# Performance work log

Measured on AMD Instinct MI355X. Metric: run time of the kernel, lower is better.

The kernel has to match this reference:

```python
import jax, jax.numpy as jnp
import numpy as np

EPS = 1e-5

def layer_norm(v, g, b):
    # torch LayerNorm: biased variance, eps inside sqrt
    m = v.mean(-1, keepdims=True)
    var = ((v - m) ** 2).mean(-1, keepdims=True)
    return (v - m) / jnp.sqrt(var + EPS) * g + b

def setup_inputs() -> dict:
    key = jax.random.key(0)
    k_q, k_x, k_w = jax.random.split(key, 3)
    B, C1, H, W = 8, 1024, 32, 32
    C2 = 32
    Cp = C1 // 4  # proj output dim = 256
    q = jax.random.normal(k_q, (B, C1, H, W), jnp.float32)
    x = jax.random.normal(k_x, (B, C2, H, W), jnp.float32)
    Wp = jax.random.normal(k_w, (Cp, C1), jnp.float32) / np.sqrt(C1).astype(np.float32)
    bp = jnp.zeros((Cp,), jnp.float32)
    g1 = jnp.ones((Cp,), jnp.float32)
    b1 = jnp.zeros((Cp,), jnp.float32)
    g2 = jnp.ones((C2,), jnp.float32)
    b2 = jnp.zeros((C2,), jnp.float32)
    return {"q": q, "x": x, "Wp": Wp, "bp": bp, "g1": g1, "b1": b1, "g2": g2, "b2": b2}

def reference(q, x, Wp, bp, g1, b1, g2, b2):
    B, C1, H, W = q.shape
    C2 = x.shape[1]
    Cp = Wp.shape[0]
    N = H * W
    qf = q.reshape(B, C1, N).transpose(0, 2, 1)   # [B, N, C1]
    xf = x.reshape(B, C2, N).transpose(0, 2, 1)   # [B, N, C2]
    qn = layer_norm(jnp.einsum('bnc,dc->bnd', qf, Wp) + bp, g1, b1)  # [B, N, Cp]
    xn = layer_norm(xf, g2, b2)                                      # [B, N, C2]
    out = jnp.einsum('bnc,bnd->bncd', qn, xn)     # [B, N, Cp, C2]
    out = out.reshape(B, N, Cp * C2).transpose(0, 2, 1).reshape(B, Cp * C2, H, W)
    return out
```

## Files before the change

kernel.cpp:

```cpp
#include <hip/hip_runtime.h>

typedef __attribute__((ext_vector_type(8))) short bf16x8;
typedef __attribute__((ext_vector_type(4))) float f32x4;

#define C1N 1024
#define CP 256
#define C2N 32
#define NPB 1024
#define BATCH 8
#define BK 64

__device__ __forceinline__ unsigned short f2bf(float f) {
  unsigned u = __float_as_uint(f);
  u += 0x7fffu + ((u >> 16) & 1u);
  return (unsigned short)(u >> 16);
}

__global__ __launch_bounds__(256) void prep_kernel(
    const float* __restrict__ x, const float* __restrict__ Wp,
    const float* __restrict__ g2, const float* __restrict__ b2,
    short* __restrict__ Wpb, float* __restrict__ xn)
{
  const int tid = threadIdx.x;
  if (blockIdx.x < 32) {
    int g = blockIdx.x * 256 + tid;
    int b = g >> 10, n = g & 1023;
    const float* xb = x + (size_t)b * C2N * NPB + n;
    float v[C2N];
    float s = 0.f;
#pragma unroll
    for (int c = 0; c < C2N; ++c) { v[c] = xb[(size_t)c * NPB]; s += v[c]; }
    float m = s * (1.0f / C2N);
    float s2 = 0.f;
#pragma unroll
    for (int c = 0; c < C2N; ++c) { float d = v[c] - m; s2 += d * d; }
    float rs = rsqrtf(s2 * (1.0f / C2N) + 1e-5f);
    float* xo = xn + (size_t)b * C2N * NPB + n;
#pragma unroll
    for (int c = 0; c < C2N; ++c) xo[(size_t)c * NPB] = (v[c] - m) * rs * g2[c] + b2[c];
  } else {
    int base = (blockIdx.x - 32) * 256 + tid;
#pragma unroll
    for (int it = 0; it < 8; ++it) {
      int pos = it * 8192 + base;
      f32x4 w = ((const f32x4*)Wp)[pos];
      ushort4 o;
      o.x = f2bf(w.x); o.y = f2bf(w.y); o.z = f2bf(w.z); o.w = f2bf(w.w);
      ((ushort4*)Wpb)[pos] = o;
    }
  }
}

__global__ __launch_bounds__(512) void gemm_ln_kernel(
    const float* __restrict__ q, const short* __restrict__ Wpb,
    const float* __restrict__ bp, const float* __restrict__ g1, const float* __restrict__ b1,
    float* __restrict__ qn)
{
  __shared__ short Wp_s[2][CP * BK];
  __shared__ float p1[8][32], p2[8][32], lm[32], lr[32];

  const int tid  = threadIdx.x;
  const int lane = tid & 63;
  const int wv   = tid >> 6;
  const int colA = lane & 15;
  const int grp  = lane >> 4;
  const int bb   = blockIdx.y;
  const int n0   = blockIdx.x * 32;

  const float* qb = q + (size_t)bb * C1N * NPB;

  f32x4 acc[2][2];
#pragma unroll
  for (int i = 0; i < 2; ++i)
#pragma unroll
    for (int j = 0; j < 2; ++j) acc[i][j] = (f32x4){0.f, 0.f, 0.f, 0.f};

  const int drow_off = lane >> 3;
  const int kslot_g  = (lane & 7) ^ drow_off;

  auto stage = [&](int buf, int ks) {
    const int k0 = ks * BK;
#pragma unroll
    for (int i = 0; i < 4; ++i) {
      int d0 = wv * 32 + i * 8;
      const short* gsrc = Wpb + (size_t)(d0 + drow_off) * C1N + k0 + kslot_g * 8;
      short* ldst = &Wp_s[buf][d0 * BK];
      __builtin_amdgcn_global_load_lds((const __attribute__((address_space(1))) void*)gsrc,
                                       (__attribute__((address_space(3))) void*)ldst,
                                       16, 0, 0);
    }
  };

  stage(0, 0);
  __syncthreads();

  for (int ks = 0; ks < C1N / BK; ++ks) {
    const int cur = ks & 1;
    if (ks < C1N / BK - 1) stage(cur ^ 1, ks + 1);

    const float* qk = qb + (size_t)(ks * BK) * NPB + n0;
#pragma unroll
    for (int kk2 = 0; kk2 < 2; ++kk2) {
      bf16x8 bfrag[2];
#pragma unroll
      for (int nf = 0; nf < 2; ++nf) {
#pragma unroll
        for (int j = 0; j < 8; ++j) {
          float v = qk[(size_t)(kk2 * 32 + grp * 8 + j) * NPB + nf * 16 + colA];
          bfrag[nf][j] = (short)f2bf(v);
        }
      }
#pragma unroll
      for (int df = 0; df < 2; ++df) {
        int row  = wv * 32 + df * 16 + colA;
        int boff = row * (BK * 2) + ((((kk2 << 2) + grp) ^ (row & 7)) << 4);
        bf16x8 afrag = *(const bf16x8*)((const char*)&Wp_s[cur][0] + boff);
        acc[df][0] = __builtin_amdgcn_mfma_f32_16x16x32_bf16(afrag, bfrag[0], acc[df][0], 0, 0, 0);
        acc[df][1] = __builtin_amdgcn_mfma_f32_16x16x32_bf16(afrag, bfrag[1], acc[df][1], 0, 0, 0);
      }
    }
    __syncthreads();
  }

  float s1[2] = {0.f, 0.f}, s2[2] = {0.f, 0.f};
#pragma unroll
  for (int df = 0; df < 2; ++df) {
#pragma unroll
    for (int r = 0; r < 4; ++r) {
      int d = wv * 32 + df * 16 + grp * 4 + r;
      float bpv = bp[d];
#pragma unroll
      for (int nf = 0; nf < 2; ++nf) {
        acc[df][nf][r] += bpv;
        float v = acc[df][nf][r];
        s1[nf] += v; s2[nf] += v * v;
      }
    }
  }
#pragma unroll
  for (int nf = 0; nf < 2; ++nf) {
    s1[nf] += __shfl_xor(s1[nf], 16); s1[nf] += __shfl_xor(s1[nf], 32);
    s2[nf] += __shfl_xor(s2[nf], 16); s2[nf] += __shfl_xor(s2[nf], 32);
  }
  if (lane < 16) {
    p1[wv][lane] = s1[0]; p1[wv][16 + lane] = s1[1];
    p2[wv][lane] = s2[0]; p2[wv][16 + lane] = s2[1];
  }
  __syncthreads();
  if (tid < 32) {
    float a1 = 0.f, a2 = 0.f;
#pragma unroll
    for (int w = 0; w < 8; ++w) { a1 += p1[w][tid]; a2 += p2[w][tid]; }
    float m  = a1 * (1.0f / CP);
    float var = a2 * (1.0f / CP) - m * m;
    lm[tid] = m;
    lr[tid] = rsqrtf(var + 1e-5f);
  }
  __syncthreads();
#pragma unroll
  for (int df = 0; df < 2; ++df) {
#pragma unroll
    for (int r = 0; r < 4; ++r) {
      int d = wv * 32 + df * 16 + grp * 4 + r;
      float gv = g1[d], bv = b1[d];
#pragma unroll
      for (int nf = 0; nf < 2; ++nf) {
        int col = nf * 16 + colA;
        float outv = (acc[df][nf][r] - lm[col]) * lr[col] * gv + bv;
        qn[((size_t)bb * CP + d) * NPB + n0 + col] = outv;
      }
    }
  }
}

__global__ __launch_bounds__(256) void outer_kernel(
    const float* __restrict__ qn, const float* __restrict__ xn, float* __restrict__ out)
{
  const int blk = blockIdx.x;
  const int bb = blk >> 8;
  const int d  = blk & 255;
  const int n4 = threadIdx.x * 4;

  const f32x4 qv = *(const f32x4*)(qn + ((size_t)bb * CP + d) * NPB + n4);
  const float* xb = xn + (size_t)bb * C2N * NPB + n4;
  float* ob = out + ((size_t)bb * (CP * C2N) + (size_t)d * C2N) * NPB + n4;

#pragma unroll 8
  for (int c = 0; c < C2N; ++c) {
    f32x4 xv = *(const f32x4*)(xb + (size_t)c * NPB);
    f32x4 ov = qv * xv;
    *(f32x4*)(ob + (size_t)c * NPB) = ov;
  }
}

extern "C" void kernel_launch(void* const* d_in, const int* in_sizes, int n_in,
                              void* d_out, int out_size, void* d_ws, size_t ws_size,
                              hipStream_t stream) {
  const float* q  = (const float*)d_in[0];
  const float* x  = (const float*)d_in[1];
  const float* Wp = (const float*)d_in[2];
  const float* bp = (const float*)d_in[3];
  const float* g1 = (const float*)d_in[4];
  const float* b1 = (const float*)d_in[5];
  const float* g2 = (const float*)d_in[6];
  const float* b2 = (const float*)d_in[7];
  float* out = (float*)d_out;

  short* Wpb = (short*)d_ws;
  float* xn  = (float*)((char*)d_ws + (512 << 10));
  float* qn  = (float*)((char*)d_ws + (512 << 10) + (1 << 20));

  prep_kernel<<<64, 256, 0, stream>>>(x, Wp, g2, b2, Wpb, xn);
  gemm_ln_kernel<<<dim3(32, 8), 512, 0, stream>>>(q, Wpb, bp, g1, b1, qn);
  outer_kernel<<<2048, 256, 0, stream>>>(qn, xn, out);
}
```

Measured before the change: 333.2 us.

## Fuse outer-product write into GEMM+LayerNorm kernel, dropping qn intermediate

The separate outer-product kernel is removed. Its work now runs in the GEMM+LN kernel's epilogue: the normalized q values stay in registers, xn tiles are staged into shared memory, and the output is written directly. This avoids writing and re-reading the qn intermediate and saves a launch. In exchange, the large output write is issued by only 256 blocks using scalar 64-byte-segment stores instead of float4 stores across 2048 blocks, which may reduce achieved write bandwidth.

```diff
diff --git a/kernel.cpp b/kernel.cpp
--- a/kernel.cpp
+++ b/kernel.cpp
@@ -2,6 +2,7 @@
 
 typedef __attribute__((ext_vector_type(8))) short bf16x8;
 typedef __attribute__((ext_vector_type(4))) float f32x4;
+typedef __attribute__((ext_vector_type(2))) float f32x2;
 
 #define C1N 1024
 #define CP 256
@@ -51,12 +52,13 @@
   }
 }
 
-__global__ __launch_bounds__(512) void gemm_ln_kernel(
+__global__ __launch_bounds__(512) void gemm_ln_outer_kernel(
     const float* __restrict__ q, const short* __restrict__ Wpb,
     const float* __restrict__ bp, const float* __restrict__ g1, const float* __restrict__ b1,
-    float* __restrict__ qn)
+    const float* __restrict__ xn, float* __restrict__ out)
 {
   __shared__ short Wp_s[2][CP * BK];
+  __shared__ float xn_s[C2N][32];
   __shared__ float p1[8][32], p2[8][32], lm[32], lr[32];
 
   const int tid  = threadIdx.x;
@@ -69,6 +71,12 @@
 
   const float* qb = q + (size_t)bb * C1N * NPB;
 
+  {
+    int c = tid >> 4, cp = (tid & 15) * 2;
+    f32x2 v = *(const f32x2*)(xn + ((size_t)bb * C2N + c) * NPB + n0 + cp);
+    xn_s[c][cp] = v.x; xn_s[c][cp + 1] = v.y;
+  }
+
   f32x4 acc[2][2];
 #pragma unroll
   for (int i = 0; i < 2; ++i)
@@ -157,6 +165,8 @@
     lr[tid] = rsqrtf(var + 1e-5f);
   }
   __syncthreads();
+
+  float qv[2][4][2];
 #pragma unroll
   for (int df = 0; df < 2; ++df) {
 #pragma unroll
@@ -166,30 +176,26 @@
 #pragma unroll
       for (int nf = 0; nf < 2; ++nf) {
         int col = nf * 16 + colA;
-        float outv = (acc[df][nf][r] - lm[col]) * lr[col] * gv + bv;
-        qn[((size_t)bb * CP + d) * NPB + n0 + col] = outv;
-      }
-    }
-  }
-}
-
-__global__ __launch_bounds__(256) void outer_kernel(
-    const float* __restrict__ qn, const float* __restrict__ xn, float* __restrict__ out)
-{
-  const int blk = blockIdx.x;
-  const int bb = blk >> 8;
-  const int d  = blk & 255;
-  const int n4 = threadIdx.x * 4;
-
-  const f32x4 qv = *(const f32x4*)(qn + ((size_t)bb * CP + d) * NPB + n4);
-  const float* xb = xn + (size_t)bb * C2N * NPB + n4;
-  float* ob = out + ((size_t)bb * (CP * C2N) + (size_t)d * C2N) * NPB + n4;
-
-#pragma unroll 8
+        qv[df][r][nf] = (acc[df][nf][r] - lm[col]) * lr[col] * gv + bv;
+      }
+    }
+  }
+
+  float* ob = out + (size_t)bb * (CP * C2N) * NPB + n0 + colA;
+#pragma unroll 4
   for (int c = 0; c < C2N; ++c) {
-    f32x4 xv = *(const f32x4*)(xb + (size_t)c * NPB);
-    f32x4 ov = qv * xv;
-    *(f32x4*)(ob + (size_t)c * NPB) = ov;
+    float xv0 = xn_s[c][colA];
+    float xv1 = xn_s[c][16 + colA];
+#pragma unroll
+    for (int df = 0; df < 2; ++df) {
+#pragma unroll
+      for (int r = 0; r < 4; ++r) {
+        int d = wv * 32 + df * 16 + grp * 4 + r;
+        float* p = ob + (size_t)(d * C2N + c) * NPB;
+        p[0]  = qv[df][r][0] * xv0;
+        p[16] = qv[df][r][1] * xv1;
+      }
+    }
   }
 }
 
@@ -208,9 +214,7 @@
 
   short* Wpb = (short*)d_ws;
   float* xn  = (float*)((char*)d_ws + (512 << 10));
-  float* qn  = (float*)((char*)d_ws + (512 << 10) + (1 << 20));
 
   prep_kernel<<<64, 256, 0, stream>>>(x, Wp, g2, b2, Wpb, xn);
-  gemm_ln_kernel<<<dim3(32, 8), 512, 0, stream>>>(q, Wpb, bp, g1, b1, qn);
-  outer_kernel<<<2048, 256, 0, stream>>>(qn, xn, out);
-}
+  gemm_ln_outer_kernel<<<dim3(32, 8), 512, 0, stream>>>(q, Wpb, bp, g1, b1, xn, out);
+}
```

After: 341.2 us. 2.4% more time.
